# Optimization experiments

Measured on AMD Instinct MI355X. Metric: run time of the kernel, lower is better.

The kernel has to match this reference:

```python
import jax, jax.numpy as jnp
import numpy as np

EMBED_DIM = 1024
NUM_HEADS = 16
HEAD_DIM = EMBED_DIM // NUM_HEADS
SCALE = HEAD_DIM ** -0.5


def setup_inputs() -> dict:
    key = jax.random.key(0)
    ks = jax.random.split(key, 11)
    B, S, D = 2, 2048, EMBED_DIM
    s = 1.0 / np.sqrt(D)
    return {
        "query": jax.random.normal(ks[0], (B, S, D), jnp.float32),
        "key": jax.random.normal(ks[1], (B, S, D), jnp.float32),
        "value": jax.random.normal(ks[2], (B, S, D), jnp.float32),
        "Wq": jax.random.normal(ks[3], (D, D), jnp.float32) * s,
        "bq": jnp.zeros((D,), jnp.float32),
        "Wk": jax.random.normal(ks[4], (D, D), jnp.float32) * s,
        "bk": jnp.zeros((D,), jnp.float32),
        "Wv": jax.random.normal(ks[5], (D, D), jnp.float32) * s,
        "bv": jnp.zeros((D,), jnp.float32),
        "Wo": jax.random.normal(ks[6], (D, D), jnp.float32) * s,
        "bo": jnp.zeros((D,), jnp.float32),
    }


def reference(query, key, value, Wq, bq, Wk, bk, Wv, bv, Wo, bo):
    B, T, D = query.shape
    S = key.shape[1]
    H, Dh = NUM_HEADS, HEAD_DIM
    # projections -> [B, H, len, Dh]
    q = (query @ Wq.T + bq).reshape(B, T, H, Dh).transpose(0, 2, 1, 3)
    k = (key @ Wk.T + bk).reshape(B, S, H, Dh).transpose(0, 2, 1, 3)
    v = (value @ Wv.T + bv).reshape(B, S, H, Dh).transpose(0, 2, 1, 3)
    scores = jnp.einsum('bhtd,bhsd->bhts', q, k) * SCALE  # [B,H,T,S]
    attn = jax.nn.sigmoid(scores)  # no row normalization; dropout=0.0 -> identity
    out = jnp.einsum('bhts,bhsd->bhtd', attn, v)  # [B,H,T,Dh]
    out = out.transpose(0, 2, 1, 3).reshape(B, T, D)
    out = out @ Wo.T + bo
    attn_weights = attn.mean(axis=1)  # [B,T,S]
    return out, attn_weights
```

## Files before the change

### kernel.cpp

```cpp
#include <hip/hip_runtime.h>
#include <hip/hip_bf16.h>


#define QH_OFF  0
#define KH_OFF  4194304
#define VT_OFF  8388608
#define OH_OFF  12582912
#define XB_OFF  16777216
#define XQB_OFF 0
#define XKB_OFF 4194304
#define XVB_OFF 8388608
#define WQB_OFF 12582912
#define WKB_OFF 13631488
#define WVB_OFF 14680064
#define WS_MIN_BYTES (16777216ull * 2ull)
#define WS_BIG_BYTES ((16777216ull + 15728640ull) * 2ull)

typedef short v8s  __attribute__((ext_vector_type(8)));
typedef unsigned short v8us __attribute__((ext_vector_type(8)));
typedef float v4f  __attribute__((ext_vector_type(4)));
typedef unsigned int v4u __attribute__((ext_vector_type(4)));

#define MFMA_BF16(a,b,c) __builtin_amdgcn_mfma_f32_16x16x32_bf16((a),(b),(c),0,0,0)

__device__ __forceinline__ float sigmoid8(float x) {
  float e = __builtin_amdgcn_exp2f(x * -0.18033688011112042f);
  return __builtin_amdgcn_rcpf(1.0f + e);
}

__device__ __forceinline__ unsigned short f2bf(float f) {
  unsigned int u = __builtin_bit_cast(unsigned int, f);
  u += 0x7FFFu + ((u >> 16) & 1u);
  return (unsigned short)(u >> 16);
}

__device__ __forceinline__ unsigned int pack2bf(float a, float b) {
  return (unsigned int)f2bf(a) | ((unsigned int)f2bf(b) << 16);
}

__global__ void cvt_inputs(const float* xq, const float* xk, const float* xv,
                           const float* wq, const float* wk, const float* wv,
                           unsigned short* __restrict__ dst)
{
  const unsigned int id = blockIdx.x * 256u + threadIdx.x;
  const float* src; unsigned int off;
  if (id < 4194304u)        { src = xq; off = id; }
  else if (id < 8388608u)   { src = xk; off = id - 4194304u; }
  else if (id < 12582912u)  { src = xv; off = id - 8388608u; }
  else if (id < 13631488u)  { src = wq; off = id - 12582912u; }
  else if (id < 14680064u)  { src = wk; off = id - 13631488u; }
  else                      { src = wv; off = id - 14680064u; }
  dst[id] = f2bf(src[off]);
}

__global__ void proj_mfma_bf16(const unsigned short* __restrict__ xb,
                               const float* bq, const float* bk, const float* bv,
                               unsigned short* __restrict__ ws)
{
  const int tid = threadIdx.x, lane = tid & 63, wv_ = tid >> 6;
  const int wm = wv_ >> 1, wn = wv_ & 1;
  const int mode = blockIdx.z;

  const unsigned short *A, *Bw; const float* bias;
  int mt, nt;
  if (mode == 0)      { A = xb + XQB_OFF; Bw = xb + WQB_OFF; bias = bq; mt = blockIdx.x; nt = blockIdx.y; }
  else if (mode == 1) { A = xb + XKB_OFF; Bw = xb + WKB_OFF; bias = bk; mt = blockIdx.x; nt = blockIdx.y; }
  else                { A = xb + WVB_OFF; Bw = xb + XVB_OFF; bias = bv;
                        int flat = blockIdx.y * 32 + blockIdx.x; mt = flat >> 5; nt = flat & 31; }
  const int m0 = mt * 128, n0 = nt * 128;

  __shared__ alignas(16) unsigned short sA[128 * 72];
  __shared__ alignas(16) unsigned short sB[128 * 72];

  const int srow = tid >> 3;
  const int scol = (tid & 7) * 8;

  v4f acc[4][4] = {};

  for (int k0 = 0; k0 < 1024; k0 += 64) {
#pragma unroll
    for (int i = 0; i < 4; i++) {
      v8us r = *(const v8us*)&A[(size_t)(m0 + i * 32 + srow) * 1024 + k0 + scol];
      *(v8us*)&sA[(i * 32 + srow) * 72 + scol] = r;
    }
#pragma unroll
    for (int i = 0; i < 4; i++) {
      v8us r = *(const v8us*)&Bw[(size_t)(n0 + i * 32 + srow) * 1024 + k0 + scol];
      *(v8us*)&sB[(i * 32 + srow) * 72 + scol] = r;
    }
    __syncthreads();

#pragma unroll
    for (int kk = 0; kk < 2; kk++) {
      v8s af[4], bfr[4];
#pragma unroll
      for (int m = 0; m < 4; m++)
        af[m] = *(const v8s*)&sA[(wm * 64 + m * 16 + (lane & 15)) * 72 + kk * 32 + (lane >> 4) * 8];
#pragma unroll
      for (int n = 0; n < 4; n++)
        bfr[n] = *(const v8s*)&sB[(wn * 64 + n * 16 + (lane & 15)) * 72 + kk * 32 + (lane >> 4) * 8];
#pragma unroll
      for (int m = 0; m < 4; m++)
#pragma unroll
        for (int n = 0; n < 4; n++)
          acc[m][n] = MFMA_BF16(af[m], bfr[n], acc[m][n]);
    }
    __syncthreads();
  }

#pragma unroll
  for (int m = 0; m < 4; m++) {
#pragma unroll
    for (int n = 0; n < 4; n++) {
      const int gn = n0 + wn * 64 + n * 16 + (lane & 15);
#pragma unroll
      for (int j = 0; j < 4; j++) {
        const int gm = m0 + wm * 64 + m * 16 + (lane >> 4) * 4 + j;
        float val = acc[m][n][j];
        if (mode == 2) {
          val += bias[gm];
          const int hh = gm >> 6, dh = gm & 63, bb = gn >> 11, ss = gn & 2047;
          ws[(size_t)VT_OFF + ((size_t)((bb * 16 + hh) * 64 + dh)) * 2048 + ss] = f2bf(val);
        } else {
          val += bias[gn];
          const int bb = gm >> 11, tt = gm & 2047, hh = gn >> 6, dh = gn & 63;
          const size_t base = (mode == 0) ? (size_t)QH_OFF : (size_t)KH_OFF;
          ws[base + ((size_t)((bb * 16 + hh) * 2048 + tt)) * 64 + dh] = f2bf(val);
        }
      }
    }
  }
}

__global__ void proj_mfma_f32(const float* xq, const float* xk, const float* xv,
                              const float* wq, const float* wk, const float* wv,
                              const float* bq, const float* bk, const float* bv,
                              unsigned short* __restrict__ ws)
{
  const int tid = threadIdx.x, lane = tid & 63, wv_ = tid >> 6;
  const int wm = wv_ >> 1, wn = wv_ & 1;
  const int mode = blockIdx.z;

  const float *Af, *Bf, *bias;
  int mt, nt;
  if (mode == 0)      { Af = xq; Bf = wq; bias = bq; mt = blockIdx.x; nt = blockIdx.y; }
  else if (mode == 1) { Af = xk; Bf = wk; bias = bk; mt = blockIdx.x; nt = blockIdx.y; }
  else                { Af = wv; Bf = xv; bias = bv;
                        int flat = blockIdx.y * 32 + blockIdx.x; mt = flat >> 6; nt = flat & 63; }
  const int m0 = mt * 128, n0 = nt * 64;

  __shared__ alignas(16) unsigned short sA[128 * 64];
  __shared__ alignas(16) unsigned short sB[64 * 64];

  v4f acc[4][2] = {};

  for (int k0 = 0; k0 < 1024; k0 += 64) {
#pragma unroll
    for (int e = 0; e < 32; e++) {
      const int idx = e * 256 + tid;
      const int row = idx >> 6, col = idx & 63;
      sA[idx] = f2bf(Af[(size_t)(m0 + row) * 1024 + k0 + col]);
    }
#pragma unroll
    for (int e = 0; e < 16; e++) {
      const int idx = e * 256 + tid;
      const int row = idx >> 6, col = idx & 63;
      sB[idx] = f2bf(Bf[(size_t)(n0 + row) * 1024 + k0 + col]);
    }
    __syncthreads();

#pragma unroll
    for (int kk = 0; kk < 2; kk++) {
      v8s af[4], bfr[2];
#pragma unroll
      for (int m = 0; m < 4; m++)
        af[m] = *(const v8s*)&sA[(wm * 64 + m * 16 + (lane & 15)) * 64 + kk * 32 + (lane >> 4) * 8];
#pragma unroll
      for (int n = 0; n < 2; n++)
        bfr[n] = *(const v8s*)&sB[(wn * 32 + n * 16 + (lane & 15)) * 64 + kk * 32 + (lane >> 4) * 8];
#pragma unroll
      for (int m = 0; m < 4; m++)
#pragma unroll
        for (int n = 0; n < 2; n++)
          acc[m][n] = MFMA_BF16(af[m], bfr[n], acc[m][n]);
    }
    __syncthreads();
  }

#pragma unroll
  for (int m = 0; m < 4; m++) {
#pragma unroll
    for (int n = 0; n < 2; n++) {
      const int gn = n0 + wn * 32 + n * 16 + (lane & 15);
#pragma unroll
      for (int j = 0; j < 4; j++) {
        const int gm = m0 + wm * 64 + m * 16 + (lane >> 4) * 4 + j;
        float val = acc[m][n][j];
        if (mode == 2) {
          val += bias[gm];
          const int hh = gm >> 6, dh = gm & 63, bb = gn >> 11, ss = gn & 2047;
          ws[(size_t)VT_OFF + ((size_t)((bb * 16 + hh) * 64 + dh)) * 2048 + ss] = f2bf(val);
        } else {
          val += bias[gn];
          const int bb = gm >> 11, tt = gm & 2047, hh = gn >> 6, dh = gn & 63;
          const size_t base = (mode == 0) ? (size_t)QH_OFF : (size_t)KH_OFF;
          ws[base + ((size_t)((bb * 16 + hh) * 2048 + tt)) * 64 + dh] = f2bf(val);
        }
      }
    }
  }
}

__global__ void attn_fused(unsigned short* __restrict__ ws,
                           float* __restrict__ aw)
{
  __shared__ alignas(16) unsigned short Ks[128 * 64];

  const int tid = threadIdx.x, lane = tid & 63, w = tid >> 6;
  const int hi = lane >> 4;
  const int srow = tid >> 3;
  const int scol = (tid & 7) * 8;
  const int sswz = scol ^ ((srow & 7) << 3);
  const int xoff = (lane & 7) << 3;

  const int hwid = blockIdx.y * 32 + blockIdx.x;

  if (hwid < 1024) {
    const int g = hwid >> 3, r = hwid & 7;
    const int bh = ((g >> 5) << 3) | r;
    const int t0 = (g & 31) * 64;
    const size_t qb = (size_t)QH_OFF + (size_t)bh * 131072;
    const size_t kb = (size_t)KH_OFF + (size_t)bh * 131072;
    const size_t vb = (size_t)VT_OFF + (size_t)bh * 131072;

    v8s qf[2];
#pragma unroll
    for (int kk = 0; kk < 2; kk++)
      qf[kk] = *(const v8s*)&ws[qb + (size_t)(t0 + w * 16 + (lane & 15)) * 64 + kk * 32 + hi * 8];

    v4f oacc[4] = {};

    for (int s0 = 0; s0 < 2048; s0 += 128) {
#pragma unroll
      for (int i = 0; i < 4; i++) {
        v8us r2 = *(const v8us*)&ws[kb + (size_t)(s0 + i * 32 + srow) * 64 + scol];
        *(v8us*)&Ks[(i * 32 + srow) * 64 + sswz] = r2;
      }
      __syncthreads();

      unsigned int pk[8][2];
#pragma unroll
      for (int nf = 0; nf < 8; nf++) {
        v4f sc = {};
#pragma unroll
        for (int kk = 0; kk < 2; kk++) {
          v8s kf = *(const v8s*)&Ks[(nf * 16 + (lane & 15)) * 64 + ((kk * 32 + hi * 8) ^ xoff)];
          sc = MFMA_BF16(kf, qf[kk], sc);
        }
        pk[nf][0] = pack2bf(sigmoid8(sc[0]), sigmoid8(sc[1]));
        pk[nf][1] = pack2bf(sigmoid8(sc[2]), sigmoid8(sc[3]));
      }

#pragma unroll
      for (int ks = 0; ks < 4; ks++) {
        v4u wrd;
#pragma unroll
        for (int wd = 0; wd < 4; wd++) {
          const int srcLane = (lane & 15) + (((2 * hi + (wd >> 1)) & 3) << 4);
          unsigned int a = __shfl(pk[2 * ks][wd & 1], srcLane);
          unsigned int b = __shfl(pk[2 * ks + 1][wd & 1], srcLane);
          wrd[wd] = (hi < 2) ? a : b;
        }
        v8s pa = __builtin_bit_cast(v8s, wrd);
#pragma unroll
        for (int nf2 = 0; nf2 < 4; nf2++) {
          v8s vf = *(const v8s*)&ws[vb + (size_t)(nf2 * 16 + (lane & 15)) * 2048 + s0 + ks * 32 + hi * 8];
          oacc[nf2] = MFMA_BF16(pa, vf, oacc[nf2]);
        }
      }
      __syncthreads();
    }

    const int b = bh >> 4, h = bh & 15;
#pragma unroll
    for (int nf = 0; nf < 4; nf++)
#pragma unroll
      for (int j = 0; j < 4; j++) {
        int t = t0 + w * 16 + hi * 4 + j;
        int dh = nf * 16 + (lane & 15);
        ws[(size_t)OH_OFF + ((size_t)(b * 2048 + t)) * 1024 + h * 64 + dh] = f2bf(oacc[nf][j]);
      }
  } else {
    const int wid = hwid - 1024;
    const int g = wid >> 3, r = wid & 7;
    const int grp = ((g >> 5) << 3) | r;
    const int t0 = (g & 31) * 64;
    const int b  = grp >> 4;
    const int s0 = (grp & 15) * 128;

    v4f macc[8] = {};

    for (int h = 0; h < 16; h++) {
      const size_t bh64 = (size_t)(b * 16 + h) * 131072;
#pragma unroll
      for (int i = 0; i < 4; i++) {
        v8us r2 = *(const v8us*)&ws[(size_t)KH_OFF + bh64 + (size_t)(s0 + i * 32 + srow) * 64 + scol];
        *(v8us*)&Ks[(i * 32 + srow) * 64 + sswz] = r2;
      }
      __syncthreads();

      v8s qf[2];
#pragma unroll
      for (int kk = 0; kk < 2; kk++)
        qf[kk] = *(const v8s*)&ws[(size_t)QH_OFF + bh64 + (size_t)(t0 + w * 16 + (lane & 15)) * 64 + kk * 32 + (lane >> 4) * 8];

#pragma unroll
      for (int nf = 0; nf < 8; nf++) {
        v4f sc = {};
#pragma unroll
        for (int kk = 0; kk < 2; kk++) {
          v8s kf = *(const v8s*)&Ks[(nf * 16 + (lane & 15)) * 64 + ((kk * 32 + (lane >> 4) * 8) ^ xoff)];
          sc = MFMA_BF16(qf[kk], kf, sc);
        }
#pragma unroll
        for (int j = 0; j < 4; j++)
          macc[nf][j] += sigmoid8(sc[j]);
      }
      __syncthreads();
    }

#pragma unroll
    for (int nf = 0; nf < 8; nf++)
#pragma unroll
      for (int j = 0; j < 4; j++) {
        int t = t0 + w * 16 + (lane >> 4) * 4 + j;
        int s = s0 + nf * 16 + (lane & 15);
        aw[((size_t)(b * 2048 + t)) * 2048 + s] = macc[nf][j] * 0.0625f;
      }
  }
}

__global__ void out_proj_mfma(const unsigned short* __restrict__ ws,
                              const float* wo, const float* bo,
                              float* __restrict__ out)
{
  const int tid = threadIdx.x, lane = tid & 63, wv_ = tid >> 6;
  const int wm = wv_ >> 1, wn = wv_ & 1;
  const int m0 = blockIdx.x * 128, n0 = blockIdx.y * 64;

  __shared__ alignas(16) unsigned short sA[128 * 72];
  __shared__ alignas(16) unsigned short sB[64 * 72];

  const int srow = tid >> 3;
  const int scol = (tid & 7) * 8;

  v4f acc[4][2] = {};

  for (int k0 = 0; k0 < 1024; k0 += 64) {
#pragma unroll
    for (int i = 0; i < 4; i++) {
      v8us r = *(const v8us*)&ws[(size_t)OH_OFF + (size_t)(m0 + i * 32 + srow) * 1024 + k0 + scol];
      *(v8us*)&sA[(i * 32 + srow) * 72 + scol] = r;
    }
#pragma unroll
    for (int e = 0; e < 16; e++) {
      const int idx = e * 256 + tid;
      const int row = idx >> 6, col = idx & 63;
      sB[row * 72 + col] = f2bf(wo[(size_t)(n0 + row) * 1024 + k0 + col]);
    }
    __syncthreads();

#pragma unroll
    for (int kk = 0; kk < 2; kk++) {
      v8s af[4], bfr[2];
#pragma unroll
      for (int m = 0; m < 4; m++)
        af[m] = *(const v8s*)&sA[(wm * 64 + m * 16 + (lane & 15)) * 72 + kk * 32 + (lane >> 4) * 8];
#pragma unroll
      for (int n = 0; n < 2; n++)
        bfr[n] = *(const v8s*)&sB[(wn * 32 + n * 16 + (lane & 15)) * 72 + kk * 32 + (lane >> 4) * 8];
#pragma unroll
      for (int m = 0; m < 4; m++)
#pragma unroll
        for (int n = 0; n < 2; n++)
          acc[m][n] = MFMA_BF16(af[m], bfr[n], acc[m][n]);
    }
    __syncthreads();
  }

#pragma unroll
  for (int m = 0; m < 4; m++) {
#pragma unroll
    for (int n = 0; n < 2; n++) {
      const int gn = n0 + wn * 32 + n * 16 + (lane & 15);
#pragma unroll
      for (int j = 0; j < 4; j++) {
        const int gm = m0 + wm * 64 + m * 16 + (lane >> 4) * 4 + j;
        out[(size_t)gm * 1024 + gn] = acc[m][n][j] + bo[gn];
      }
    }
  }
}

extern "C" void kernel_launch(void* const* d_in, const int* in_sizes, int n_in,
                              void* d_out, int out_size, void* d_ws, size_t ws_size,
                              hipStream_t stream)
{
  const float* q  = (const float*)d_in[0];
  const float* k  = (const float*)d_in[1];
  const float* v  = (const float*)d_in[2];
  const float* Wq = (const float*)d_in[3];
  const float* bq = (const float*)d_in[4];
  const float* Wk = (const float*)d_in[5];
  const float* bk = (const float*)d_in[6];
  const float* Wv = (const float*)d_in[7];
  const float* bv = (const float*)d_in[8];
  const float* Wo = (const float*)d_in[9];
  const float* bo = (const float*)d_in[10];
  float* out = (float*)d_out;
  unsigned short* ws = (unsigned short*)d_ws;

  if (ws_size < WS_MIN_BYTES) return;

  if (ws_size >= WS_BIG_BYTES) {
    unsigned short* xb = ws + XB_OFF;
    cvt_inputs<<<61440, 256, 0, stream>>>(q, k, v, Wq, Wk, Wv, xb);
    proj_mfma_bf16<<<dim3(32, 8, 3), 256, 0, stream>>>(xb, bq, bk, bv, ws);
  } else {
    proj_mfma_f32<<<dim3(32, 16, 3), 256, 0, stream>>>(q, k, v, Wq, Wk, Wv,
                                                       bq, bk, bv, ws);
  }
  attn_fused<<<dim3(32, 64), 256, 0, stream>>>(ws, out + 4194304);
  out_proj_mfma<<<dim3(32, 16), 256, 0, stream>>>(ws, Wo, bo, out);
}
```

Baseline: 293.7 us.

## Double query rows per wave in attention blocks to reuse K and V fragments

Each attention block now covers 128 query rows instead of 64, so every wave computes two 16-row tiles (A and B) that share the K fragments loaded from LDS and the V fragments loaded from global memory. The number of attention blocks is halved and the grid shrinks from 64 to 48 rows, while the attention-weights blocks stay the same. This cuts redundant K staging and V global loads per output row, at the cost of more registers per thread and fewer blocks available to fill the GPU.

```diff
diff --git a/kernel.cpp b/kernel.cpp
--- a/kernel.cpp
+++ b/kernel.cpp
@@ -225,20 +225,22 @@
 
   const int hwid = blockIdx.y * 32 + blockIdx.x;
 
-  if (hwid < 1024) {
+  if (hwid < 512) {
     const int g = hwid >> 3, r = hwid & 7;
-    const int bh = ((g >> 5) << 3) | r;
-    const int t0 = (g & 31) * 64;
+    const int bh = ((g >> 4) << 3) | r;
+    const int t0 = (g & 15) * 128;
     const size_t qb = (size_t)QH_OFF + (size_t)bh * 131072;
     const size_t kb = (size_t)KH_OFF + (size_t)bh * 131072;
     const size_t vb = (size_t)VT_OFF + (size_t)bh * 131072;
 
-    v8s qf[2];
-#pragma unroll
-    for (int kk = 0; kk < 2; kk++)
-      qf[kk] = *(const v8s*)&ws[qb + (size_t)(t0 + w * 16 + (lane & 15)) * 64 + kk * 32 + hi * 8];
-
-    v4f oacc[4] = {};
+    v8s qfA[2], qfB[2];
+#pragma unroll
+    for (int kk = 0; kk < 2; kk++) {
+      qfA[kk] = *(const v8s*)&ws[qb + (size_t)(t0 + w * 32 + (lane & 15)) * 64 + kk * 32 + hi * 8];
+      qfB[kk] = *(const v8s*)&ws[qb + (size_t)(t0 + w * 32 + 16 + (lane & 15)) * 64 + kk * 32 + hi * 8];
+    }
+
+    v4f oaccA[4] = {}, oaccB[4] = {};
 
     for (int s0 = 0; s0 < 2048; s0 += 128) {
 #pragma unroll
@@ -248,34 +250,42 @@
       }
       __syncthreads();
 
-      unsigned int pk[8][2];
+      unsigned int pkA[8][2], pkB[8][2];
 #pragma unroll
       for (int nf = 0; nf < 8; nf++) {
-        v4f sc = {};
+        v4f scA = {}, scB = {};
 #pragma unroll
         for (int kk = 0; kk < 2; kk++) {
           v8s kf = *(const v8s*)&Ks[(nf * 16 + (lane & 15)) * 64 + ((kk * 32 + hi * 8) ^ xoff)];
-          sc = MFMA_BF16(kf, qf[kk], sc);
-        }
-        pk[nf][0] = pack2bf(sigmoid8(sc[0]), sigmoid8(sc[1]));
-        pk[nf][1] = pack2bf(sigmoid8(sc[2]), sigmoid8(sc[3]));
+          scA = MFMA_BF16(kf, qfA[kk], scA);
+          scB = MFMA_BF16(kf, qfB[kk], scB);
+        }
+        pkA[nf][0] = pack2bf(sigmoid8(scA[0]), sigmoid8(scA[1]));
+        pkA[nf][1] = pack2bf(sigmoid8(scA[2]), sigmoid8(scA[3]));
+        pkB[nf][0] = pack2bf(sigmoid8(scB[0]), sigmoid8(scB[1]));
+        pkB[nf][1] = pack2bf(sigmoid8(scB[2]), sigmoid8(scB[3]));
       }
 
 #pragma unroll
       for (int ks = 0; ks < 4; ks++) {
-        v4u wrd;
+        v4u wrdA, wrdB;
 #pragma unroll
         for (int wd = 0; wd < 4; wd++) {
           const int srcLane = (lane & 15) + (((2 * hi + (wd >> 1)) & 3) << 4);
-          unsigned int a = __shfl(pk[2 * ks][wd & 1], srcLane);
-          unsigned int b = __shfl(pk[2 * ks + 1][wd & 1], srcLane);
-          wrd[wd] = (hi < 2) ? a : b;
-        }
-        v8s pa = __builtin_bit_cast(v8s, wrd);
+          unsigned int aA = __shfl(pkA[2 * ks][wd & 1], srcLane);
+          unsigned int bA = __shfl(pkA[2 * ks + 1][wd & 1], srcLane);
+          wrdA[wd] = (hi < 2) ? aA : bA;
+          unsigned int aB = __shfl(pkB[2 * ks][wd & 1], srcLane);
+          unsigned int bB = __shfl(pkB[2 * ks + 1][wd & 1], srcLane);
+          wrdB[wd] = (hi < 2) ? aB : bB;
+        }
+        v8s paA = __builtin_bit_cast(v8s, wrdA);
+        v8s paB = __builtin_bit_cast(v8s, wrdB);
 #pragma unroll
         for (int nf2 = 0; nf2 < 4; nf2++) {
           v8s vf = *(const v8s*)&ws[vb + (size_t)(nf2 * 16 + (lane & 15)) * 2048 + s0 + ks * 32 + hi * 8];
-          oacc[nf2] = MFMA_BF16(pa, vf, oacc[nf2]);
+          oaccA[nf2] = MFMA_BF16(paA, vf, oaccA[nf2]);
+          oaccB[nf2] = MFMA_BF16(paB, vf, oaccB[nf2]);
         }
       }
       __syncthreads();
@@ -286,12 +296,14 @@
     for (int nf = 0; nf < 4; nf++)
 #pragma unroll
       for (int j = 0; j < 4; j++) {
-        int t = t0 + w * 16 + hi * 4 + j;
-        int dh = nf * 16 + (lane & 15);
-        ws[(size_t)OH_OFF + ((size_t)(b * 2048 + t)) * 1024 + h * 64 + dh] = f2bf(oacc[nf][j]);
+        const int dh = nf * 16 + (lane & 15);
+        int tA = t0 + w * 32 + hi * 4 + j;
+        ws[(size_t)OH_OFF + ((size_t)(b * 2048 + tA)) * 1024 + h * 64 + dh] = f2bf(oaccA[nf][j]);
+        int tB = tA + 16;
+        ws[(size_t)OH_OFF + ((size_t)(b * 2048 + tB)) * 1024 + h * 64 + dh] = f2bf(oaccB[nf][j]);
       }
   } else {
-    const int wid = hwid - 1024;
+    const int wid = hwid - 512;
     const int g = wid >> 3, r = wid & 7;
     const int grp = ((g >> 5) << 3) | r;
     const int t0 = (g & 31) * 64;
@@ -430,6 +442,6 @@
     proj_mfma_f32<<<dim3(32, 16, 3), 256, 0, stream>>>(q, k, v, Wq, Wk, Wv,
                                                        bq, bk, bv, ws);
   }
-  attn_fused<<<dim3(32, 64), 256, 0, stream>>>(ws, out + 4194304);
+  attn_fused<<<dim3(32, 48), 256, 0, stream>>>(ws, out + 4194304);
   out_proj_mfma<<<dim3(32, 16), 256, 0, stream>>>(ws, Wo, bo, out);
 }
```

Measured after the change: 242.8 us. 17.3% less time.
